# Performance work log

Measured on AMD Instinct MI355X. Metric: run time of the kernel, lower is better.

Reference implementation:

```python
import jax, jax.numpy as jnp
import numpy as np

N_NODES = 50000
N_EDGES = 800000
NFEAT = 256
NHID = 128
NCLASS = 64
LEAKY_SLOPE = 0.01  # torch F.leaky_relu default


def setup_inputs() -> dict:
    key = jax.random.key(0)
    ks = jax.random.split(key, 7)
    x = jax.random.normal(ks[0], (N_NODES, NFEAT), dtype=jnp.float32)
    edge_src = jax.random.randint(ks[1], (N_EDGES,), 0, N_NODES)
    edge_dst = jax.random.randint(ks[2], (N_EDGES,), 0, N_NODES)
    edge_w = jax.random.uniform(ks[3], (N_EDGES,), dtype=jnp.float32)
    W1 = jax.random.normal(ks[4], (NFEAT, NHID), dtype=jnp.float32) * (1.0 / np.sqrt(NFEAT))
    W2 = jax.random.normal(ks[5], (NHID, NHID), dtype=jnp.float32) * (1.0 / np.sqrt(NHID))
    W3 = jax.random.uniform(ks[6], (NHID, NCLASS), dtype=jnp.float32,
                            minval=-1.0 / np.sqrt(NCLASS), maxval=1.0 / np.sqrt(NCLASS))
    return {"x": x, "edge_src": edge_src, "edge_dst": edge_dst, "edge_w": edge_w,
            "W1": W1, "W2": W2, "W3": W3}


def reference(x, edge_src, edge_dst, edge_w, W1, W2, W3):
    n = x.shape[0]

    def spmm(h):
        # sparse adj @ h via gather + weighted scatter-add over edges
        msgs = h[edge_src] * edge_w[:, None]           # [E, d]
        return jax.ops.segment_sum(msgs, edge_dst, num_segments=n)

    x1 = jax.nn.leaky_relu(spmm(x @ W1), negative_slope=LEAKY_SLOPE)  # gc1 + leaky_relu
    x3 = spmm(x1 @ W2)                                                # gc2
    Y = jax.nn.sigmoid(x3 @ W3)                                       # multilabel head
    return (Y, x3)
```

## Files before the change

### kernel.cpp

```cpp
#include <hip/hip_runtime.h>
#include <hip/hip_bf16.h>


constexpr int N_NODES = 50000;
constexpr int N_EDGES = 800000;
constexpr int NFEAT = 256;
constexpr int NHID = 128;
constexpr int NCLASS = 64;
constexpr int EW = 64;

typedef __attribute__((ext_vector_type(8))) short short8;
typedef __attribute__((ext_vector_type(4))) float f32x4;

__device__ __forceinline__ unsigned short f32_to_bf16_rne(float f) {
  unsigned u = __float_as_uint(f);
  unsigned r = u + 0x7fffu + ((u >> 16) & 1u);
  return (unsigned short)(r >> 16);
}
__device__ __forceinline__ float bf16_to_f32(unsigned short s) {
  return __uint_as_float(((unsigned)s) << 16);
}

template <int K, int N>
__device__ __forceinline__ void pack_dev(const float* __restrict__ W,
                                         short* __restrict__ Bh,
                                         short* __restrict__ Bl, int blk) {
  int idx = blk * 256 + threadIdx.x;
  constexpr int NFRAG = (K / 32) * (N / 16);
  if (idx >= NFRAG * 64) return;
  int l = idx & 63;
  int f = idx >> 6;
  int kb = f / (N / 16), nt = f % (N / 16);
  int g = l >> 4;
  int n = nt * 16 + (l & 15);
#pragma unroll
  for (int j = 0; j < 8; ++j) {
    int k = kb * 32 + g * 8 + j;
    float v = W[(size_t)k * N + n];
    unsigned short h = f32_to_bf16_rne(v);
    float rem = v - bf16_to_f32(h);
    Bh[((size_t)f * 64 + l) * 8 + j] = (short)h;
    Bl[((size_t)f * 64 + l) * 8 + j] = (short)f32_to_bf16_rne(rem);
  }
}

__global__ __launch_bounds__(256) void pack_all(const float* __restrict__ W1,
                                                const float* __restrict__ W2,
                                                const float* __restrict__ W3,
                                                short* W1h, short* W1l, short* W2h,
                                                short* W2l, short* W3h, short* W3l) {
  int b = blockIdx.x;
  if (b < 16) pack_dev<NFEAT, NHID>(W1, W1h, W1l, b);
  else if (b < 24) pack_dev<NHID, NHID>(W2, W2h, W2l, b - 16);
  else pack_dev<NHID, NCLASS>(W3, W3h, W3l, b - 24);
}

template <int K, int N, bool A_BF16, bool SIGMOID, bool OUT_BF16>
__global__ __launch_bounds__(256) void gemm_mfma(const void* __restrict__ Av,
                                                 const short* __restrict__ Bh,
                                                 const short* __restrict__ Bl,
                                                 void* __restrict__ Cv, int M) {
  constexpr int WCOL = N / 2;
  constexpr int F = WCOL / 16;
  const int tid = threadIdx.x;
  const int wid = tid >> 6;
  const int lane = tid & 63;
  const int g = lane >> 4;
  const int brow = blockIdx.x * 32 + (wid >> 1) * 16;
  const int col0 = (wid & 1) * WCOL;
  const int row_a = brow + (lane & 15);

  f32x4 acc[F];
#pragma unroll
  for (int i = 0; i < F; ++i) acc[i] = (f32x4){0.f, 0.f, 0.f, 0.f};

#pragma unroll
  for (int kb = 0; kb < K / 32; ++kb) {
    const int ca = kb * 32 + g * 8;
    short8 ah, al;
    if (A_BF16) {
      const unsigned short* A = (const unsigned short*)Av;
      if (row_a < M) {
        ah = *reinterpret_cast<const short8*>(A + (size_t)row_a * K + ca);
      } else {
        ah = (short8){0, 0, 0, 0, 0, 0, 0, 0};
      }
    } else {
      const float* A = (const float*)Av;
      float4 a0 = {0.f, 0.f, 0.f, 0.f}, a1 = {0.f, 0.f, 0.f, 0.f};
      if (row_a < M) {
        a0 = *reinterpret_cast<const float4*>(A + (size_t)row_a * K + ca);
        a1 = *reinterpret_cast<const float4*>(A + (size_t)row_a * K + ca + 4);
      }
      float av[8] = {a0.x, a0.y, a0.z, a0.w, a1.x, a1.y, a1.z, a1.w};
#pragma unroll
      for (int j = 0; j < 8; ++j) {
        float v = av[j];
        unsigned short h = f32_to_bf16_rne(v);
        ah[j] = (short)h;
        al[j] = (short)f32_to_bf16_rne(v - bf16_to_f32(h));
      }
    }
#pragma unroll
    for (int nt = 0; nt < F; ++nt) {
      int f = kb * (N / 16) + (col0 >> 4) + nt;
      short8 bh = *reinterpret_cast<const short8*>(Bh + ((size_t)f * 64 + lane) * 8);
      short8 bl = *reinterpret_cast<const short8*>(Bl + ((size_t)f * 64 + lane) * 8);
      acc[nt] = __builtin_amdgcn_mfma_f32_16x16x32_bf16(ah, bh, acc[nt], 0, 0, 0);
      if (!A_BF16)
        acc[nt] = __builtin_amdgcn_mfma_f32_16x16x32_bf16(al, bh, acc[nt], 0, 0, 0);
      acc[nt] = __builtin_amdgcn_mfma_f32_16x16x32_bf16(ah, bl, acc[nt], 0, 0, 0);
    }
  }

#pragma unroll
  for (int nt = 0; nt < F; ++nt) {
    int c = col0 + nt * 16 + (lane & 15);
#pragma unroll
    for (int reg = 0; reg < 4; ++reg) {
      int r = brow + g * 4 + reg;
      if (r < M) {
        float v = acc[nt][reg];
        if (SIGMOID) v = 1.f / (1.f + __expf(-v));
        if (OUT_BF16) {
          ((unsigned short*)Cv)[(size_t)r * N + c] = f32_to_bf16_rne(v);
        } else {
          ((float*)Cv)[(size_t)r * N + c] = v;
        }
      }
    }
  }
}

__global__ __launch_bounds__(256) void ell_fill(const int* __restrict__ src,
                                                const int* __restrict__ dst,
                                                const float* __restrict__ w,
                                                int* __restrict__ cnt,
                                                float2* __restrict__ ell, int nE) {
  int e = blockIdx.x * 256 + threadIdx.x;
  if (e >= nE) return;
  int d = dst[e];
  int slot = atomicAdd(&cnt[d], 1);
  if (slot < EW) {
    float2 p;
    p.x = __int_as_float(src[e]);
    p.y = w[e];
    ell[(size_t)d * EW + slot] = p;
  }
}

template <bool LEAKY, bool OUT_BF16>
__global__ __launch_bounds__(256) void spmm_ell(const unsigned* __restrict__ hb,
                                                const float2* __restrict__ ell,
                                                const int* __restrict__ cnt,
                                                void* __restrict__ outv, int nNodes) {
  int node = blockIdx.x * 4 + (threadIdx.x >> 6);
  if (node >= nNodes) return;
  int lane = threadIdx.x & 63;
  int n = cnt[node];
  if (n > EW) n = EW;
  const float2* row = ell + (size_t)node * EW;
  float ax = 0.f, ay = 0.f;
  int j = 0;
  for (; j + 4 <= n; j += 4) {
    float2 e0 = row[j], e1 = row[j + 1], e2 = row[j + 2], e3 = row[j + 3];
    unsigned u0 = hb[(size_t)__float_as_int(e0.x) * 64 + lane];
    unsigned u1 = hb[(size_t)__float_as_int(e1.x) * 64 + lane];
    unsigned u2 = hb[(size_t)__float_as_int(e2.x) * 64 + lane];
    unsigned u3 = hb[(size_t)__float_as_int(e3.x) * 64 + lane];
    ax += e0.y * __uint_as_float(u0 << 16);
    ay += e0.y * __uint_as_float(u0 & 0xffff0000u);
    ax += e1.y * __uint_as_float(u1 << 16);
    ay += e1.y * __uint_as_float(u1 & 0xffff0000u);
    ax += e2.y * __uint_as_float(u2 << 16);
    ay += e2.y * __uint_as_float(u2 & 0xffff0000u);
    ax += e3.y * __uint_as_float(u3 << 16);
    ay += e3.y * __uint_as_float(u3 & 0xffff0000u);
  }
  for (; j < n; ++j) {
    float2 e0 = row[j];
    unsigned u0 = hb[(size_t)__float_as_int(e0.x) * 64 + lane];
    ax += e0.y * __uint_as_float(u0 << 16);
    ay += e0.y * __uint_as_float(u0 & 0xffff0000u);
  }
  if (LEAKY) {
    ax = (ax > 0.f) ? ax : 0.01f * ax;
    ay = (ay > 0.f) ? ay : 0.01f * ay;
  }
  if (OUT_BF16) {
    unsigned pk = ((unsigned)f32_to_bf16_rne(ay) << 16) | (unsigned)f32_to_bf16_rne(ax);
    ((unsigned*)outv)[(size_t)node * 64 + lane] = pk;
  } else {
    float2 o;
    o.x = ax;
    o.y = ay;
    ((float2*)outv)[(size_t)node * 64 + lane] = o;
  }
}

extern "C" void kernel_launch(void* const* d_in, const int* in_sizes, int n_in,
                              void* d_out, int out_size, void* d_ws, size_t ws_size,
                              hipStream_t stream) {
  const float* x = (const float*)d_in[0];
  const int* edge_src = (const int*)d_in[1];
  const int* edge_dst = (const int*)d_in[2];
  const float* edge_w = (const float*)d_in[3];
  const float* W1 = (const float*)d_in[4];
  const float* W2 = (const float*)d_in[5];
  const float* W3 = (const float*)d_in[6];

  float* Y = (float*)d_out;
  float* x3 = (float*)d_out + (size_t)N_NODES * NCLASS;

  unsigned* hb = (unsigned*)d_ws;
  unsigned* x1b = hb + (size_t)N_NODES * 64;
  float2* ell = (float2*)(x1b + (size_t)N_NODES * 64);
  int* cnt = (int*)(ell + (size_t)N_NODES * EW);
  short* W1h = (short*)(cnt + N_NODES);
  short* W1l = W1h + NFEAT * NHID;
  short* W2h = W1l + NFEAT * NHID;
  short* W2l = W2h + NHID * NHID;
  short* W3h = W2l + NHID * NHID;
  short* W3l = W3h + NHID * NCLASS;

  const int gemm_grid = (N_NODES + 31) / 32;
  const int edge_grid = (N_EDGES + 255) / 256;
  const int node_grid = (N_NODES + 3) / 4;

  pack_all<<<28, 256, 0, stream>>>(W1, W2, W3, W1h, W1l, W2h, W2l, W3h, W3l);

  hipMemsetAsync(cnt, 0, (size_t)N_NODES * sizeof(int), stream);
  ell_fill<<<edge_grid, 256, 0, stream>>>(edge_src, edge_dst, edge_w, cnt, ell, N_EDGES);

  gemm_mfma<NFEAT, NHID, false, false, true>
      <<<gemm_grid, 256, 0, stream>>>(x, W1h, W1l, hb, N_NODES);

  spmm_ell<true, true><<<node_grid, 256, 0, stream>>>(hb, ell, cnt, x1b, N_NODES);

  gemm_mfma<NHID, NHID, true, false, true>
      <<<gemm_grid, 256, 0, stream>>>(x1b, W2h, W2l, hb, N_NODES);

  spmm_ell<false, false><<<node_grid, 256, 0, stream>>>(hb, ell, cnt, x3, N_NODES);

  gemm_mfma<NHID, NCLASS, false, true, false>
      <<<gemm_grid, 256, 0, stream>>>(x3, W3h, W3l, Y, N_NODES);
}
```

Baseline: 281.7 us.

## Fuse weight packing with count reset, co-schedule GEMM1 with ELL fill, shuffle edge descriptors

```diff
diff --git a/kernel.cpp b/kernel.cpp
--- a/kernel.cpp
+++ b/kernel.cpp
@@ -38,35 +38,42 @@
     int k = kb * 32 + g * 8 + j;
     float v = W[(size_t)k * N + n];
     unsigned short h = f32_to_bf16_rne(v);
-    float rem = v - bf16_to_f32(h);
     Bh[((size_t)f * 64 + l) * 8 + j] = (short)h;
-    Bl[((size_t)f * 64 + l) * 8 + j] = (short)f32_to_bf16_rne(rem);
-  }
-}
-
-__global__ __launch_bounds__(256) void pack_all(const float* __restrict__ W1,
-                                                const float* __restrict__ W2,
-                                                const float* __restrict__ W3,
-                                                short* W1h, short* W1l, short* W2h,
-                                                short* W2l, short* W3h, short* W3l) {
+    Bl[((size_t)f * 64 + l) * 8 + j] = (short)f32_to_bf16_rne(v - bf16_to_f32(h));
+  }
+}
+
+__global__ __launch_bounds__(256) void prep(const float* __restrict__ W1,
+                                            const float* __restrict__ W2,
+                                            const float* __restrict__ W3,
+                                            short* W1h, short* W1l, short* W2h,
+                                            short* W2l, short* W3h, short* W3l,
+                                            int* __restrict__ cnt) {
   int b = blockIdx.x;
-  if (b < 16) pack_dev<NFEAT, NHID>(W1, W1h, W1l, b);
-  else if (b < 24) pack_dev<NHID, NHID>(W2, W2h, W2l, b - 16);
-  else pack_dev<NHID, NCLASS>(W3, W3h, W3l, b - 24);
+  if (b < 196) {
+    int i = b * 256 + threadIdx.x;
+    if (i < N_NODES) cnt[i] = 0;
+  } else if (b < 212) {
+    pack_dev<NFEAT, NHID>(W1, W1h, W1l, b - 196);
+  } else if (b < 220) {
+    pack_dev<NHID, NHID>(W2, W2h, W2l, b - 212);
+  } else {
+    pack_dev<NHID, NCLASS>(W3, W3h, W3l, b - 220);
+  }
 }
 
 template <int K, int N, bool A_BF16, bool SIGMOID, bool OUT_BF16>
-__global__ __launch_bounds__(256) void gemm_mfma(const void* __restrict__ Av,
-                                                 const short* __restrict__ Bh,
-                                                 const short* __restrict__ Bl,
-                                                 void* __restrict__ Cv, int M) {
+__device__ __forceinline__ void gemm_body(int bx, const void* __restrict__ Av,
+                                          const short* __restrict__ Bh,
+                                          const short* __restrict__ Bl,
+                                          void* __restrict__ Cv, int M) {
   constexpr int WCOL = N / 2;
   constexpr int F = WCOL / 16;
   const int tid = threadIdx.x;
   const int wid = tid >> 6;
   const int lane = tid & 63;
   const int g = lane >> 4;
-  const int brow = blockIdx.x * 32 + (wid >> 1) * 16;
+  const int brow = bx * 32 + (wid >> 1) * 16;
   const int col0 = (wid & 1) * WCOL;
   const int row_a = brow + (lane & 15);
 
@@ -132,20 +139,36 @@
   }
 }
 
-__global__ __launch_bounds__(256) void ell_fill(const int* __restrict__ src,
-                                                const int* __restrict__ dst,
-                                                const float* __restrict__ w,
-                                                int* __restrict__ cnt,
-                                                float2* __restrict__ ell, int nE) {
-  int e = blockIdx.x * 256 + threadIdx.x;
-  if (e >= nE) return;
-  int d = dst[e];
-  int slot = atomicAdd(&cnt[d], 1);
-  if (slot < EW) {
-    float2 p;
-    p.x = __int_as_float(src[e]);
-    p.y = w[e];
-    ell[(size_t)d * EW + slot] = p;
+template <int K, int N, bool A_BF16, bool SIGMOID, bool OUT_BF16>
+__global__ __launch_bounds__(256) void gemm_mfma(const void* __restrict__ Av,
+                                                 const short* __restrict__ Bh,
+                                                 const short* __restrict__ Bl,
+                                                 void* __restrict__ Cv, int M) {
+  gemm_body<K, N, A_BF16, SIGMOID, OUT_BF16>(blockIdx.x, Av, Bh, Bl, Cv, M);
+}
+
+constexpr int GB1 = (N_NODES + 31) / 32;
+
+__global__ __launch_bounds__(256) void fused_gemm1_fill(
+    const float* __restrict__ x, const short* __restrict__ W1h,
+    const short* __restrict__ W1l, unsigned short* __restrict__ hb,
+    const int* __restrict__ src, const int* __restrict__ dst,
+    const float* __restrict__ w, int* __restrict__ cnt,
+    float2* __restrict__ ell) {
+  int b = blockIdx.x;
+  if (b < GB1) {
+    gemm_body<NFEAT, NHID, false, false, true>(b, x, W1h, W1l, hb, N_NODES);
+  } else {
+    int e = (b - GB1) * 256 + threadIdx.x;
+    if (e >= N_EDGES) return;
+    int d = dst[e];
+    int slot = atomicAdd(&cnt[d], 1);
+    if (slot < EW) {
+      float2 p;
+      p.x = __int_as_float(src[e]);
+      p.y = w[e];
+      ell[(size_t)d * EW + slot] = p;
+    }
   }
 }
 
@@ -159,30 +182,35 @@
   int lane = threadIdx.x & 63;
   int n = cnt[node];
   if (n > EW) n = EW;
-  const float2* row = ell + (size_t)node * EW;
+  float2 mydesc = ell[(size_t)node * EW + lane];
+  int msrc = __float_as_int(mydesc.x);
+  float mw = mydesc.y;
+
   float ax = 0.f, ay = 0.f;
   int j = 0;
-  for (; j + 4 <= n; j += 4) {
-    float2 e0 = row[j], e1 = row[j + 1], e2 = row[j + 2], e3 = row[j + 3];
-    unsigned u0 = hb[(size_t)__float_as_int(e0.x) * 64 + lane];
-    unsigned u1 = hb[(size_t)__float_as_int(e1.x) * 64 + lane];
-    unsigned u2 = hb[(size_t)__float_as_int(e2.x) * 64 + lane];
-    unsigned u3 = hb[(size_t)__float_as_int(e3.x) * 64 + lane];
-    ax += e0.y * __uint_as_float(u0 << 16);
-    ay += e0.y * __uint_as_float(u0 & 0xffff0000u);
-    ax += e1.y * __uint_as_float(u1 << 16);
-    ay += e1.y * __uint_as_float(u1 & 0xffff0000u);
-    ax += e2.y * __uint_as_float(u2 << 16);
-    ay += e2.y * __uint_as_float(u2 & 0xffff0000u);
-    ax += e3.y * __uint_as_float(u3 << 16);
-    ay += e3.y * __uint_as_float(u3 & 0xffff0000u);
+  for (; j + 8 <= n; j += 8) {
+    unsigned u[8];
+    float ww[8];
+#pragma unroll
+    for (int t = 0; t < 8; ++t) {
+      int s = __shfl(msrc, j + t, 64);
+      ww[t] = __shfl(mw, j + t, 64);
+      u[t] = hb[(size_t)s * 64 + lane];
+    }
+#pragma unroll
+    for (int t = 0; t < 8; ++t) {
+      ax += ww[t] * __uint_as_float(u[t] << 16);
+      ay += ww[t] * __uint_as_float(u[t] & 0xffff0000u);
+    }
   }
   for (; j < n; ++j) {
-    float2 e0 = row[j];
-    unsigned u0 = hb[(size_t)__float_as_int(e0.x) * 64 + lane];
-    ax += e0.y * __uint_as_float(u0 << 16);
-    ay += e0.y * __uint_as_float(u0 & 0xffff0000u);
-  }
+    int s = __shfl(msrc, j, 64);
+    float wwj = __shfl(mw, j, 64);
+    unsigned uj = hb[(size_t)s * 64 + lane];
+    ax += wwj * __uint_as_float(uj << 16);
+    ay += wwj * __uint_as_float(uj & 0xffff0000u);
+  }
+
   if (LEAKY) {
     ax = (ax > 0.f) ? ax : 0.01f * ax;
     ay = (ay > 0.f) ? ay : 0.01f * ay;
@@ -223,17 +251,14 @@
   short* W3h = W2l + NHID * NHID;
   short* W3l = W3h + NHID * NCLASS;
 
+  const int edge_blocks = (N_EDGES + 255) / 256;
+  const int node_grid = (N_NODES + 3) / 4;
   const int gemm_grid = (N_NODES + 31) / 32;
-  const int edge_grid = (N_EDGES + 255) / 256;
-  const int node_grid = (N_NODES + 3) / 4;
-
-  pack_all<<<28, 256, 0, stream>>>(W1, W2, W3, W1h, W1l, W2h, W2l, W3h, W3l);
-
-  hipMemsetAsync(cnt, 0, (size_t)N_NODES * sizeof(int), stream);
-  ell_fill<<<edge_grid, 256, 0, stream>>>(edge_src, edge_dst, edge_w, cnt, ell, N_EDGES);
-
-  gemm_mfma<NFEAT, NHID, false, false, true>
-      <<<gemm_grid, 256, 0, stream>>>(x, W1h, W1l, hb, N_NODES);
+
+  prep<<<224, 256, 0, stream>>>(W1, W2, W3, W1h, W1l, W2h, W2l, W3h, W3l, cnt);
+
+  fused_gemm1_fill<<<GB1 + edge_blocks, 256, 0, stream>>>(
+      x, W1h, W1l, (unsigned short*)hb, edge_src, edge_dst, edge_w, cnt, ell);
 
   spmm_ell<true, true><<<node_grid, 256, 0, stream>>>(hb, ell, cnt, x1b, N_NODES);
 
```

New measurement: 258.6 us. 1.09x faster.
